# Kernel optimization log

Measured on AMD Instinct MI355X. Metric: run time of the kernel, lower is better.

Reference implementation:

```python
import jax, jax.numpy as jnp
import numpy as np

NUM_HEADS = 16

def alibi_slopes(num_heads):
    # 1 / ((2**8)**(1/H))**(i+1) for i in range(H)  -> shape (H, 1, 1)
    x = (2.0 ** 8) ** (1.0 / num_heads)
    return (1.0 / x ** (jnp.arange(1, num_heads + 1, dtype=jnp.float32)))[:, None, None]

def setup_inputs() -> dict:
    key = jax.random.key(0)
    k1, k2, k3 = jax.random.split(key, 3)
    B, T, D = 4, 2048, 1024
    x = jax.random.normal(k1, (B, T, D), dtype=jnp.float32)
    w_qkv = jax.random.normal(k2, (D, 3 * D), dtype=jnp.float32) * 0.02
    w_o = jax.random.normal(k3, (D, D), dtype=jnp.float32) * 0.02
    return {"x": x, "w_qkv": w_qkv, "w_o": w_o}

def reference(x, w_qkv, w_o):
    B, T, C = x.shape
    H = NUM_HEADS
    dh = C // H
    qkv = x @ w_qkv                                   # [B, T, 3C]
    q, k, v = jnp.split(qkv, 3, axis=-1)
    # b t (h d) -> b h t d
    q = q.reshape(B, T, H, dh).transpose(0, 2, 1, 3)
    k = k.reshape(B, T, H, dh).transpose(0, 2, 1, 3)
    v = v.reshape(B, T, H, dh).transpose(0, 2, 1, 3)
    wei = jnp.einsum('bhqd,bhkd->bhqk', q, k)         # [B, H, T, T]
    rel = (jnp.arange(T)[None, :] - jnp.arange(T)[:, None]).astype(jnp.float32)
    bias = alibi_slopes(H) * rel                      # [H, T, T]
    scale = jnp.float32(C) ** 0.5                     # note: full dim C, as in source
    scores = wei / scale + bias
    causal = jnp.tril(jnp.ones((T, T), dtype=bool))
    scores = jnp.where(causal, scores, jnp.float32(-jnp.inf))
    attn = jax.nn.softmax(scores, axis=-1)
    out = jnp.einsum('bhqk,bhkd->bhqd', attn, v)      # [B, H, T, dh]
    concat = out.transpose(0, 2, 1, 3).reshape(B, T, C)
    return concat @ w_o
```

## Files before the change

kernel.cpp:

```cpp
#include <hip/hip_runtime.h>
#include <hip/hip_bf16.h>

typedef float f32x4 __attribute__((ext_vector_type(4)));
typedef short bf16x8 __attribute__((ext_vector_type(8)));
typedef short bf16x4 __attribute__((ext_vector_type(4)));

static __device__ __forceinline__ short f2bs(float f) {
  __hip_bfloat16 h = __float2bfloat16(f);
  union { __hip_bfloat16 h; short s; } u;
  u.h = h;
  return u.s;
}

#define GLDS(gp, lp) __builtin_amdgcn_global_load_lds( \
    (const __attribute__((address_space(1))) unsigned int*)(gp), \
    (__attribute__((address_space(3))) unsigned int*)(lp), 16, 0, 0)

__global__ __launch_bounds__(256) void cvt_f32_bf16(const float* __restrict__ in,
                                                    short* __restrict__ out, int n4) {
  int i = blockIdx.x * 256 + threadIdx.x;
  if (i >= n4) return;
  f32x4 v = ((const f32x4*)in)[i];
  bf16x4 o;
  o[0] = f2bs(v[0]); o[1] = f2bs(v[1]); o[2] = f2bs(v[2]); o[3] = f2bs(v[3]);
  ((bf16x4*)out)[i] = o;
}

__global__ __launch_bounds__(256) void transpose_cvt(const float* __restrict__ in,
                                                     short* __restrict__ out,
                                                     int R, int C) {
  __shared__ float tile[32][33];
  int bx = blockIdx.x * 32;
  int by = blockIdx.y * 32;
  int tx = threadIdx.x & 31;
  int ty = threadIdx.x >> 5;
#pragma unroll
  for (int i = 0; i < 32; i += 8)
    tile[ty + i][tx] = in[(long)(by + ty + i) * C + bx + tx];
  __syncthreads();
#pragma unroll
  for (int i = 0; i < 32; i += 8)
    out[(long)(bx + ty + i) * R + by + tx] = f2bs(tile[tx][ty + i]);
}

__device__ __forceinline__ void gemm_compute_tile(const short* Ac, const short* Bc,
                                                  int r0, int c0, int lr, int quad,
                                                  f32x4 acc[4][4]) {
  bf16x8 af[4], bfr[4];
#pragma unroll
  for (int i = 0; i < 4; ++i)
    af[i] = *(const bf16x8*)(Ac + (r0 + i * 16 + lr) * 32 + quad * 8);
#pragma unroll
  for (int j = 0; j < 4; ++j)
    bfr[j] = *(const bf16x8*)(Bc + (c0 + j * 16 + lr) * 32 + quad * 8);
#pragma unroll
  for (int i = 0; i < 4; ++i)
#pragma unroll
    for (int j = 0; j < 4; ++j)
      acc[i][j] = __builtin_amdgcn_mfma_f32_16x16x32_bf16(af[i], bfr[j], acc[i][j], 0, 0, 0);
}

__device__ __forceinline__ void gemm_mainloop(const short* __restrict__ A,
                                              const short* __restrict__ Bt,
                                              int K, int rowA0, int rowB0,
                                              short* As, short* Bs,
                                              f32x4 acc[4][4]) {
  const int tid = threadIdx.x;
  const int wave = tid >> 6;
  const int lane = tid & 63;
  const int lr = lane & 15;
  const int quad = lane >> 4;
  const short* aP = A + (long)(rowA0 + wave * 32 + (lane >> 2)) * K + (lane & 3) * 8;
  const short* bP = Bt + (long)(rowB0 + wave * 32 + (lane >> 2)) * K + (lane & 3) * 8;
  const int woff = wave * 32 * 32;
  const int r0 = (wave >> 1) * 64;
  const int c0 = (wave & 1) * 64;
  const int c16K = 16 * K;
  const int BUF = 128 * 32;
  GLDS(aP, As + woff);
  GLDS(aP + c16K, As + woff + 16 * 32);
  GLDS(bP, Bs + woff);
  GLDS(bP + c16K, Bs + woff + 16 * 32);
  aP += 32; bP += 32;
  const int nIter = K >> 5;
#pragma unroll 1
  for (int i = 0; i < nIter; i += 2) {
    __syncthreads();
    if (i + 1 < nIter) {
      GLDS(aP, As + BUF + woff);
      GLDS(aP + c16K, As + BUF + woff + 16 * 32);
      GLDS(bP, Bs + BUF + woff);
      GLDS(bP + c16K, Bs + BUF + woff + 16 * 32);
      aP += 32; bP += 32;
    }
    gemm_compute_tile(As, Bs, r0, c0, lr, quad, acc);
    __syncthreads();
    if (i + 2 < nIter) {
      GLDS(aP, As + woff);
      GLDS(aP + c16K, As + woff + 16 * 32);
      GLDS(bP, Bs + woff);
      GLDS(bP + c16K, Bs + woff + 16 * 32);
      aP += 32; bP += 32;
    }
    gemm_compute_tile(As + BUF, Bs + BUF, r0, c0, lr, quad, acc);
  }
}

__global__ __launch_bounds__(256, 5) void gemm_qkv(const short* __restrict__ xb,
                                                   const short* __restrict__ wT,
                                                   short* __restrict__ q,
                                                   short* __restrict__ k,
                                                   short* __restrict__ vt) {
  __shared__ __align__(16) short As[2 * 128 * 32];
  __shared__ __align__(16) short Bs[2 * 128 * 32];
  f32x4 acc[4][4];
#pragma unroll
  for (int i = 0; i < 4; ++i)
#pragma unroll
    for (int j = 0; j < 4; ++j)
      acc[i][j] = (f32x4){0.f, 0.f, 0.f, 0.f};
  const int tileM = blockIdx.x * 128;
  const int tileN = blockIdx.y * 128;
  gemm_mainloop(xb, wT, 1024, tileM, tileN, As, Bs, acc);
  const int tid = threadIdx.x;
  const int wave = tid >> 6;
  const int lane = tid & 63;
  const int lr = lane & 15;
  const int quad = lane >> 4;
#pragma unroll
  for (int i = 0; i < 4; ++i) {
    const int row0 = tileM + (wave >> 1) * 64 + i * 16 + quad * 4;
    const int b = row0 >> 11;
    const int t = row0 & 2047;
#pragma unroll
    for (int j = 0; j < 4; ++j) {
      int col = tileN + (wave & 1) * 64 + j * 16 + lr;
      int region = col >> 10;
      int w = col & 1023;
      int h = w >> 6;
      int d = w & 63;
      long bh = (long)b * 16 + h;
      if (region == 0) {
#pragma unroll
        for (int r = 0; r < 4; ++r)
          q[(bh * 2048 + t + r) * 64 + d] = f2bs(acc[i][j][r] * 0.03125f);
      } else if (region == 1) {
#pragma unroll
        for (int r = 0; r < 4; ++r)
          k[(bh * 2048 + t + r) * 64 + d] = f2bs(acc[i][j][r]);
      } else {
        bf16x4 pk;
#pragma unroll
        for (int r = 0; r < 4; ++r) pk[r] = f2bs(acc[i][j][r]);
        *(bf16x4*)(vt + (bh * 64 + d) * 2048 + t) = pk;
      }
    }
  }
}

__global__ __launch_bounds__(256, 5) void attn(const short* __restrict__ q,
                                               const short* __restrict__ kk,
                                               const short* __restrict__ vt,
                                               short* __restrict__ cat) {
  __shared__ __align__(16) short Ks[64 * 72];
  __shared__ __align__(16) short Vs[64 * 72];
  __shared__ __align__(16) short Ps[4 * 16 * 72];
  const int bx = blockIdx.x;
  const int j = 31 - (bx >> 6);
  const int bh = bx & 63;
  const int h = bh & 15;
  const int b = bh >> 4;
  const int tid = threadIdx.x;
  const int wave = tid >> 6;
  const int lane = tid & 63;
  const int lr = lane & 15;
  const int quad = lane >> 4;
  const float l2e = 1.44269504f;
  const float slope = exp2f(-0.5f * (float)(h + 1));
  const float slope_l2e = slope * l2e;
  const float c2 = -2.0f * l2e;
  const int d_cut = (int)ceilf(20.0f * exp2f(0.5f * (float)(h + 1)));
  const short* kbg = kk + (long)bh * 2048 * 64;
  const short* vbg = vt + (long)bh * 64 * 2048;
  const int srow = tid >> 3;
  const int scol = (tid & 7) * 8;
  short* pw = Ps + wave * 16 * 72;

  const int q0 = j * 64;
  const int mrow0 = q0 + wave * 16;
  const int kt_start = max(0, (q0 - d_cut) >> 6);
  const short* qptr = q + ((long)bh * 2048 + mrow0) * 64;
  bf16x8 qf0 = *(const bf16x8*)(qptr + (long)lr * 64 + quad * 8);
  bf16x8 qf1 = *(const bf16x8*)(qptr + (long)lr * 64 + 32 + quad * 8);
  float lp = 0.f;
  f32x4 O[4];
#pragma unroll
  for (int dt = 0; dt < 4; ++dt) O[dt] = (f32x4){0.f, 0.f, 0.f, 0.f};

  const short* kg = kbg + (long)kt_start * 64 * 64;
  const short* vg = vbg + kt_start * 64;
  bf16x8 pk0 = *(const bf16x8*)(kg + srow * 64 + scol);
  bf16x8 pk1 = *(const bf16x8*)(kg + (srow + 32) * 64 + scol);
  bf16x8 pv0 = *(const bf16x8*)(vg + (long)srow * 2048 + scol);
  bf16x8 pv1 = *(const bf16x8*)(vg + (long)(srow + 32) * 2048 + scol);
  for (int kt = kt_start; kt <= j; ++kt) {
    *(bf16x8*)(Ks + srow * 72 + scol) = pk0;
    *(bf16x8*)(Ks + (srow + 32) * 72 + scol) = pk1;
    *(bf16x8*)(Vs + srow * 72 + scol) = pv0;
    *(bf16x8*)(Vs + (srow + 32) * 72 + scol) = pv1;
    __syncthreads();
    if (kt < j) {
      const short* kg2 = kbg + (long)(kt + 1) * 64 * 64;
      const short* vg2 = vbg + (kt + 1) * 64;
      pk0 = *(const bf16x8*)(kg2 + srow * 64 + scol);
      pk1 = *(const bf16x8*)(kg2 + (srow + 32) * 64 + scol);
      pv0 = *(const bf16x8*)(vg2 + (long)srow * 2048 + scol);
      pv1 = *(const bf16x8*)(vg2 + (long)(srow + 32) * 2048 + scol);
    }
    const int kbase = kt * 64;
    f32x4 S[4];
#pragma unroll
    for (int ct = 0; ct < 4; ++ct) {
      bf16x8 kf0 = *(const bf16x8*)(Ks + (ct * 16 + lr) * 72 + quad * 8);
      bf16x8 kf1 = *(const bf16x8*)(Ks + (ct * 16 + lr) * 72 + 32 + quad * 8);
      f32x4 a = (f32x4){0.f, 0.f, 0.f, 0.f};
      a = __builtin_amdgcn_mfma_f32_16x16x32_bf16(kf0, qf0, a, 0, 0, 0);
      a = __builtin_amdgcn_mfma_f32_16x16x32_bf16(kf1, qf1, a, 0, 0, 0);
      S[ct] = a;
    }
    const bool diag = (kt == j);
    const float dbase = (float)(kbase - mrow0 - lr + quad * 4);
#pragma unroll
    for (int ct = 0; ct < 4; ++ct) {
      bf16x4 pkt;
#pragma unroll
      for (int r = 0; r < 4; ++r) {
        float dist = dbase + (float)(ct * 16 + r);
        float arg = fmaf(S[ct][r], l2e, fmaf(slope_l2e, dist, c2));
        if (diag) arg = (dist <= 0.f) ? arg : -10000.0f;
        float p = exp2f(arg);
        lp += p;
        pkt[r] = f2bs(p);
      }
      *(bf16x4*)(pw + lr * 72 + ct * 16 + quad * 4) = pkt;
    }
    asm volatile("s_waitcnt lgkmcnt(0)" ::: "memory");
    bf16x8 pf0 = *(const bf16x8*)(pw + lr * 72 + quad * 8);
    bf16x8 pf1 = *(const bf16x8*)(pw + lr * 72 + 32 + quad * 8);
#pragma unroll
    for (int dt = 0; dt < 4; ++dt) {
      bf16x8 vf0 = *(const bf16x8*)(Vs + (dt * 16 + lr) * 72 + quad * 8);
      bf16x8 vf1 = *(const bf16x8*)(Vs + (dt * 16 + lr) * 72 + 32 + quad * 8);
      O[dt] = __builtin_amdgcn_mfma_f32_16x16x32_bf16(pf0, vf0, O[dt], 0, 0, 0);
      O[dt] = __builtin_amdgcn_mfma_f32_16x16x32_bf16(pf1, vf1, O[dt], 0, 0, 0);
    }
    __syncthreads();
  }
  lp += __shfl_xor(lp, 16);
  lp += __shfl_xor(lp, 32);
#pragma unroll
  for (int r = 0; r < 4; ++r) {
    float lm = __shfl(lp, quad * 4 + r);
    float inv = 1.0f / lm;
    int t = mrow0 + quad * 4 + r;
#pragma unroll
    for (int dt = 0; dt < 4; ++dt)
      cat[((long)b * 2048 + t) * 1024 + h * 64 + dt * 16 + lr] =
          f2bs(O[dt][r] * inv);
  }
}

__global__ __launch_bounds__(256, 5) void gemm_out(const short* __restrict__ cat,
                                                   const short* __restrict__ woT,
                                                   float* __restrict__ out) {
  __shared__ __align__(16) short As[2 * 128 * 32];
  __shared__ __align__(16) short Bs[2 * 128 * 32];
  f32x4 acc[4][4];
#pragma unroll
  for (int i = 0; i < 4; ++i)
#pragma unroll
    for (int j = 0; j < 4; ++j)
      acc[i][j] = (f32x4){0.f, 0.f, 0.f, 0.f};
  const int tileM = blockIdx.x * 128;
  const int tileN = blockIdx.y * 128;
  gemm_mainloop(cat, woT, 1024, tileM, tileN, As, Bs, acc);
  const int tid = threadIdx.x;
  const int wave = tid >> 6;
  const int lane = tid & 63;
  const int lr = lane & 15;
  const int quad = lane >> 4;
#pragma unroll
  for (int i = 0; i < 4; ++i)
#pragma unroll
    for (int j = 0; j < 4; ++j) {
      int col = tileN + (wave & 1) * 64 + j * 16 + lr;
#pragma unroll
      for (int r = 0; r < 4; ++r) {
        int row = tileM + (wave >> 1) * 64 + i * 16 + quad * 4 + r;
        out[(long)row * 1024 + col] = acc[i][j][r];
      }
    }
}

extern "C" void kernel_launch(void* const* d_in, const int* in_sizes, int n_in,
                              void* d_out, int out_size, void* d_ws, size_t ws_size,
                              hipStream_t stream) {
  const float* x = (const float*)d_in[0];
  const float* w_qkv = (const float*)d_in[1];
  const float* w_o = (const float*)d_in[2];
  float* out = (float*)d_out;
  short* ws = (short*)d_ws;
  short* xb = ws;
  short* wqkvT = xb + 8388608;
  short* woT = wqkvT + 3145728;
  short* q = woT + 1048576;
  short* kb = q + 8388608;
  short* vt = kb + 8388608;

  cvt_f32_bf16<<<8192, 256, 0, stream>>>(x, xb, 2097152);
  transpose_cvt<<<dim3(96, 32), 256, 0, stream>>>(w_qkv, wqkvT, 1024, 3072);
  transpose_cvt<<<dim3(32, 32), 256, 0, stream>>>(w_o, woT, 1024, 1024);
  gemm_qkv<<<dim3(64, 24), 256, 0, stream>>>(xb, wqkvT, q, kb, vt);
  attn<<<dim3(2048), 256, 0, stream>>>(q, kb, vt, xb );
  gemm_out<<<dim3(64, 8), 256, 0, stream>>>(xb, woT, out);
}
```

Baseline: 265.4 us.

## Load GEMM B fragments directly to registers and precompute ALiBi bias increments

The GEMM mainloop stops staging the B (weight) tile through LDS. Each wave now loads its B fragments straight from global memory into registers, double-buffered across k-steps, while A keeps the LDS path. This removes the B shared-memory traffic and half the LDS footprint, at the cost of more registers (launch bounds drop from 5 to 3 waves per SIMD) and uncoalesced or duplicated global B reads across waves. The attention kernel also precomputes per-element ALiBi bias values that advance by a constant each tile and a causal mask bitmask, replacing per-element distance arithmetic.

```diff
diff --git a/kernel.cpp b/kernel.cpp
--- a/kernel.cpp
+++ b/kernel.cpp
@@ -43,16 +43,13 @@
     out[(long)(bx + ty + i) * R + by + tx] = f2bs(tile[tx][ty + i]);
 }
 
-__device__ __forceinline__ void gemm_compute_tile(const short* Ac, const short* Bc,
-                                                  int r0, int c0, int lr, int quad,
+__device__ __forceinline__ void gemm_compute_tile(const short* Ac, const bf16x8 bfr[4],
+                                                  int r0, int lr, int quad,
                                                   f32x4 acc[4][4]) {
-  bf16x8 af[4], bfr[4];
+  bf16x8 af[4];
 #pragma unroll
   for (int i = 0; i < 4; ++i)
     af[i] = *(const bf16x8*)(Ac + (r0 + i * 16 + lr) * 32 + quad * 8);
-#pragma unroll
-  for (int j = 0; j < 4; ++j)
-    bfr[j] = *(const bf16x8*)(Bc + (c0 + j * 16 + lr) * 32 + quad * 8);
 #pragma unroll
   for (int i = 0; i < 4; ++i)
 #pragma unroll
@@ -63,7 +60,7 @@
 __device__ __forceinline__ void gemm_mainloop(const short* __restrict__ A,
                                               const short* __restrict__ Bt,
                                               int K, int rowA0, int rowB0,
-                                              short* As, short* Bs,
+                                              short* As,
                                               f32x4 acc[4][4]) {
   const int tid = threadIdx.x;
   const int wave = tid >> 6;
@@ -71,48 +68,56 @@
   const int lr = lane & 15;
   const int quad = lane >> 4;
   const short* aP = A + (long)(rowA0 + wave * 32 + (lane >> 2)) * K + (lane & 3) * 8;
-  const short* bP = Bt + (long)(rowB0 + wave * 32 + (lane >> 2)) * K + (lane & 3) * 8;
-  const int woff = wave * 32 * 32;
+  short* aL0 = As + wave * 32 * 32;
+  short* aL1 = As + 128 * 32 + wave * 32 * 32;
   const int r0 = (wave >> 1) * 64;
-  const int c0 = (wave & 1) * 64;
   const int c16K = 16 * K;
-  const int BUF = 128 * 32;
-  GLDS(aP, As + woff);
-  GLDS(aP + c16K, As + woff + 16 * 32);
-  GLDS(bP, Bs + woff);
-  GLDS(bP + c16K, Bs + woff + 16 * 32);
-  aP += 32; bP += 32;
+  const short* bBase = Bt + (long)(rowB0 + (wave & 1) * 64 + lr) * K + quad * 8;
+  GLDS(aP, aL0);
+  GLDS(aP + c16K, aL0 + 16 * 32);
+  aP += 32;
+  bf16x8 bc[4], bn[4];
+#pragma unroll
+  for (int j = 0; j < 4; ++j)
+    bc[j] = *(const bf16x8*)(bBase + j * c16K);
   const int nIter = K >> 5;
 #pragma unroll 1
   for (int i = 0; i < nIter; i += 2) {
     __syncthreads();
     if (i + 1 < nIter) {
-      GLDS(aP, As + BUF + woff);
-      GLDS(aP + c16K, As + BUF + woff + 16 * 32);
-      GLDS(bP, Bs + BUF + woff);
-      GLDS(bP + c16K, Bs + BUF + woff + 16 * 32);
-      aP += 32; bP += 32;
-    }
-    gemm_compute_tile(As, Bs, r0, c0, lr, quad, acc);
+      GLDS(aP, aL1);
+      GLDS(aP + c16K, aL1 + 16 * 32);
+      aP += 32;
+    }
+    {
+      int k1 = (i + 1 < nIter) ? (i + 1) * 32 : 0;
+#pragma unroll
+      for (int j = 0; j < 4; ++j)
+        bn[j] = *(const bf16x8*)(bBase + j * c16K + k1);
+    }
+    gemm_compute_tile(As + wave * 0 + 0 * 0 + 0, bc, r0, lr, quad, acc);
     __syncthreads();
     if (i + 2 < nIter) {
-      GLDS(aP, As + woff);
-      GLDS(aP + c16K, As + woff + 16 * 32);
-      GLDS(bP, Bs + woff);
-      GLDS(bP + c16K, Bs + woff + 16 * 32);
-      aP += 32; bP += 32;
-    }
-    gemm_compute_tile(As + BUF, Bs + BUF, r0, c0, lr, quad, acc);
+      GLDS(aP, aL0);
+      GLDS(aP + c16K, aL0 + 16 * 32);
+      aP += 32;
+    }
+    {
+      int k2 = (i + 2 < nIter) ? (i + 2) * 32 : 0;
+#pragma unroll
+      for (int j = 0; j < 4; ++j)
+        bc[j] = *(const bf16x8*)(bBase + j * c16K + k2);
+    }
+    gemm_compute_tile(As + 128 * 32, bn, r0, lr, quad, acc);
   }
 }
 
-__global__ __launch_bounds__(256, 5) void gemm_qkv(const short* __restrict__ xb,
+__global__ __launch_bounds__(256, 3) void gemm_qkv(const short* __restrict__ xb,
                                                    const short* __restrict__ wT,
                                                    short* __restrict__ q,
                                                    short* __restrict__ k,
                                                    short* __restrict__ vt) {
   __shared__ __align__(16) short As[2 * 128 * 32];
-  __shared__ __align__(16) short Bs[2 * 128 * 32];
   f32x4 acc[4][4];
 #pragma unroll
   for (int i = 0; i < 4; ++i)
@@ -121,7 +126,7 @@
       acc[i][j] = (f32x4){0.f, 0.f, 0.f, 0.f};
   const int tileM = blockIdx.x * 128;
   const int tileN = blockIdx.y * 128;
-  gemm_mainloop(xb, wT, 1024, tileM, tileN, As, Bs, acc);
+  gemm_mainloop(xb, wT, 1024, tileM, tileN, As, acc);
   const int tid = threadIdx.x;
   const int wave = tid >> 6;
   const int lane = tid & 63;
@@ -196,6 +201,17 @@
   f32x4 O[4];
 #pragma unroll
   for (int dt = 0; dt < 4; ++dt) O[dt] = (f32x4){0.f, 0.f, 0.f, 0.f};
+  float bias[4][4];
+  unsigned okbits = 0;
+#pragma unroll
+  for (int ct = 0; ct < 4; ++ct)
+#pragma unroll
+    for (int r = 0; r < 4; ++r) {
+      int off = ct * 16 + quad * 4 + r;
+      bias[ct][r] = slope_l2e * (float)(kt_start * 64 + off - mrow0 - lr) + c2;
+      if (off - wave * 16 - lr <= 0) okbits |= 1u << (ct * 4 + r);
+    }
+  const float bstep = slope_l2e * 64.0f;
 
   const short* kg = kbg + (long)kt_start * 64 * 64;
   const short* vg = vbg + kt_start * 64;
@@ -217,7 +233,6 @@
       pv0 = *(const bf16x8*)(vg2 + (long)srow * 2048 + scol);
       pv1 = *(const bf16x8*)(vg2 + (long)(srow + 32) * 2048 + scol);
     }
-    const int kbase = kt * 64;
     f32x4 S[4];
 #pragma unroll
     for (int ct = 0; ct < 4; ++ct) {
@@ -229,18 +244,17 @@
       S[ct] = a;
     }
     const bool diag = (kt == j);
-    const float dbase = (float)(kbase - mrow0 - lr + quad * 4);
 #pragma unroll
     for (int ct = 0; ct < 4; ++ct) {
       bf16x4 pkt;
 #pragma unroll
       for (int r = 0; r < 4; ++r) {
-        float dist = dbase + (float)(ct * 16 + r);
-        float arg = fmaf(S[ct][r], l2e, fmaf(slope_l2e, dist, c2));
-        if (diag) arg = (dist <= 0.f) ? arg : -10000.0f;
+        float arg = fmaf(S[ct][r], l2e, bias[ct][r]);
+        if (diag && !(okbits & (1u << (ct * 4 + r)))) arg = -10000.0f;
         float p = exp2f(arg);
         lp += p;
         pkt[r] = f2bs(p);
+        bias[ct][r] += bstep;
       }
       *(bf16x4*)(pw + lr * 72 + ct * 16 + quad * 4) = pkt;
     }
@@ -270,11 +284,10 @@
   }
 }
 
-__global__ __launch_bounds__(256, 5) void gemm_out(const short* __restrict__ cat,
+__global__ __launch_bounds__(256, 3) void gemm_out(const short* __restrict__ cat,
                                                    const short* __restrict__ woT,
                                                    float* __restrict__ out) {
   __shared__ __align__(16) short As[2 * 128 * 32];
-  __shared__ __align__(16) short Bs[2 * 128 * 32];
   f32x4 acc[4][4];
 #pragma unroll
   for (int i = 0; i < 4; ++i)
@@ -283,7 +296,7 @@
       acc[i][j] = (f32x4){0.f, 0.f, 0.f, 0.f};
   const int tileM = blockIdx.x * 128;
   const int tileN = blockIdx.y * 128;
-  gemm_mainloop(cat, woT, 1024, tileM, tileN, As, Bs, acc);
+  gemm_mainloop(cat, woT, 1024, tileM, tileN, As, acc);
   const int tid = threadIdx.x;
   const int wave = tid >> 6;
   const int lane = tid & 63;
```

Result: slower. 326.4 us (+23.0%).

## Enlarge QKV GEMM tile to 256 rows and precompute ALiBi bias in attention

Applied to the files above, without the earlier changes.

The QKV projection GEMM now uses 512-thread blocks covering a 256x128 output tile, with an inlined double-buffered main loop that loads two A sub-tiles per wave. Each B tile fetched from the weight matrix is therefore reused across twice as many rows, cutting global traffic for B and halving the grid. Separately, the attention kernel precomputes the per-element ALiBi bias and the diagonal causal mask bits once, then advances the bias by a fixed step per key tile, which removes integer-to-float conversions and compares from the inner loop. The trade-off is more registers (a 16-float bias array) and a larger shared-memory footprint per GEMM block, which may lower occupancy.

```diff
diff --git a/kernel.cpp b/kernel.cpp
--- a/kernel.cpp
+++ b/kernel.cpp
@@ -106,12 +106,12 @@
   }
 }
 
-__global__ __launch_bounds__(256, 5) void gemm_qkv(const short* __restrict__ xb,
+__global__ __launch_bounds__(512, 4) void gemm_qkv(const short* __restrict__ xb,
                                                    const short* __restrict__ wT,
                                                    short* __restrict__ q,
                                                    short* __restrict__ k,
                                                    short* __restrict__ vt) {
-  __shared__ __align__(16) short As[2 * 128 * 32];
+  __shared__ __align__(16) short As[2 * 256 * 32];
   __shared__ __align__(16) short Bs[2 * 128 * 32];
   f32x4 acc[4][4];
 #pragma unroll
@@ -119,22 +119,55 @@
 #pragma unroll
     for (int j = 0; j < 4; ++j)
       acc[i][j] = (f32x4){0.f, 0.f, 0.f, 0.f};
-  const int tileM = blockIdx.x * 128;
+  const int tileM = blockIdx.x * 256;
   const int tileN = blockIdx.y * 128;
-  gemm_mainloop(xb, wT, 1024, tileM, tileN, As, Bs, acc);
+  const int K = 1024;
   const int tid = threadIdx.x;
   const int wave = tid >> 6;
   const int lane = tid & 63;
   const int lr = lane & 15;
   const int quad = lane >> 4;
+  const int wrow = wave >> 1;
+  const int wcol = wave & 1;
+  const short* aP1 = xb + (long)(tileM + wave * 16 + (lane >> 2)) * K + (lane & 3) * 8;
+  const short* aP2 = aP1 + (long)128 * K;
+  const short* bP  = wT + (long)(tileN + wave * 16 + (lane >> 2)) * K + (lane & 3) * 8;
+  const int woff = wave * 16 * 32;
+  const int ABUF = 256 * 32, BBUF = 128 * 32;
+  const int r0 = wrow * 64;
+  const int c0 = wcol * 64;
+  GLDS(aP1, As + woff);
+  GLDS(aP2, As + 128 * 32 + woff);
+  GLDS(bP, Bs + woff);
+  aP1 += 32; aP2 += 32; bP += 32;
+  const int nIter = K >> 5;
+#pragma unroll 1
+  for (int i = 0; i < nIter; i += 2) {
+    __syncthreads();
+    if (i + 1 < nIter) {
+      GLDS(aP1, As + ABUF + woff);
+      GLDS(aP2, As + ABUF + 128 * 32 + woff);
+      GLDS(bP, Bs + BBUF + woff);
+      aP1 += 32; aP2 += 32; bP += 32;
+    }
+    gemm_compute_tile(As, Bs, r0, c0, lr, quad, acc);
+    __syncthreads();
+    if (i + 2 < nIter) {
+      GLDS(aP1, As + woff);
+      GLDS(aP2, As + 128 * 32 + woff);
+      GLDS(bP, Bs + woff);
+      aP1 += 32; aP2 += 32; bP += 32;
+    }
+    gemm_compute_tile(As + ABUF, Bs + BBUF, r0, c0, lr, quad, acc);
+  }
 #pragma unroll
   for (int i = 0; i < 4; ++i) {
-    const int row0 = tileM + (wave >> 1) * 64 + i * 16 + quad * 4;
+    const int row0 = tileM + wrow * 64 + i * 16 + quad * 4;
     const int b = row0 >> 11;
     const int t = row0 & 2047;
 #pragma unroll
     for (int j = 0; j < 4; ++j) {
-      int col = tileN + (wave & 1) * 64 + j * 16 + lr;
+      int col = tileN + wcol * 64 + j * 16 + lr;
       int region = col >> 10;
       int w = col & 1023;
       int h = w >> 6;
@@ -196,6 +229,17 @@
   f32x4 O[4];
 #pragma unroll
   for (int dt = 0; dt < 4; ++dt) O[dt] = (f32x4){0.f, 0.f, 0.f, 0.f};
+  float bias[4][4];
+  unsigned okbits = 0;
+#pragma unroll
+  for (int ct = 0; ct < 4; ++ct)
+#pragma unroll
+    for (int r = 0; r < 4; ++r) {
+      int off = ct * 16 + quad * 4 + r;
+      bias[ct][r] = slope_l2e * (float)(kt_start * 64 + off - mrow0 - lr) + c2;
+      if (off - wave * 16 - lr <= 0) okbits |= 1u << (ct * 4 + r);
+    }
+  const float bstep = slope_l2e * 64.0f;
 
   const short* kg = kbg + (long)kt_start * 64 * 64;
   const short* vg = vbg + kt_start * 64;
@@ -217,7 +261,6 @@
       pv0 = *(const bf16x8*)(vg2 + (long)srow * 2048 + scol);
       pv1 = *(const bf16x8*)(vg2 + (long)(srow + 32) * 2048 + scol);
     }
-    const int kbase = kt * 64;
     f32x4 S[4];
 #pragma unroll
     for (int ct = 0; ct < 4; ++ct) {
@@ -229,18 +272,17 @@
       S[ct] = a;
     }
     const bool diag = (kt == j);
-    const float dbase = (float)(kbase - mrow0 - lr + quad * 4);
 #pragma unroll
     for (int ct = 0; ct < 4; ++ct) {
       bf16x4 pkt;
 #pragma unroll
       for (int r = 0; r < 4; ++r) {
-        float dist = dbase + (float)(ct * 16 + r);
-        float arg = fmaf(S[ct][r], l2e, fmaf(slope_l2e, dist, c2));
-        if (diag) arg = (dist <= 0.f) ? arg : -10000.0f;
+        float arg = fmaf(S[ct][r], l2e, bias[ct][r]);
+        if (diag && !(okbits & (1u << (ct * 4 + r)))) arg = -10000.0f;
         float p = exp2f(arg);
         lp += p;
         pkt[r] = f2bs(p);
+        bias[ct][r] += bstep;
       }
       *(bf16x4*)(pw + lr * 72 + ct * 16 + quad * 4) = pkt;
     }
@@ -320,7 +362,7 @@
   cvt_f32_bf16<<<8192, 256, 0, stream>>>(x, xb, 2097152);
   transpose_cvt<<<dim3(96, 32), 256, 0, stream>>>(w_qkv, wqkvT, 1024, 3072);
   transpose_cvt<<<dim3(32, 32), 256, 0, stream>>>(w_o, woT, 1024, 1024);
-  gemm_qkv<<<dim3(64, 24), 256, 0, stream>>>(xb, wqkvT, q, kb, vt);
+  gemm_qkv<<<dim3(32, 24), 512, 0, stream>>>(xb, wqkvT, q, kb, vt);
   attn<<<dim3(2048), 256, 0, stream>>>(q, kb, vt, xb );
   gemm_out<<<dim3(64, 8), 256, 0, stream>>>(xb, woT, out);
 }
```

Result: no change. 262.9 us (-0.9%).
